# Kernel optimization log

Hardware: AMD Instinct MI355X
Metric: run time of the kernel (lower is better)

## Reference

```python
import jax, jax.numpy as jnp
import numpy as np

N_ATOMS = 100000
N_PAIRS = 3200000
N_PROP = 16
N_BASIS = 10
W = 16  # MLP width for pp/pi/ii nodes


def setup_inputs() -> dict:
    key = jax.random.key(0)
    ks = jax.random.split(key, 16)
    s = 0.1
    inp = {
        "ind_2": jax.random.randint(ks[0], (N_PAIRS, 2), 0, N_ATOMS),
        "p1": jax.random.normal(ks[1], (N_ATOMS, N_PROP), dtype=jnp.float32),
        "basis": jax.random.normal(ks[2], (N_PAIRS, N_BASIS), dtype=jnp.float32),
        # pp_pre: [16,16], bias=True
        "Wpre0": jax.random.normal(ks[3], (N_PROP, W), dtype=jnp.float32) * s,
        "bpre0": jnp.zeros((W,), dtype=jnp.float32),
        "Wpre1": jax.random.normal(ks[4], (W, W), dtype=jnp.float32) * s,
        "bpre1": jnp.zeros((W,), dtype=jnp.float32),
        # pi: input 2*W -> W -> W*n_basis, bias=True
        "Wpi0": jax.random.normal(ks[5], (2 * W, W), dtype=jnp.float32) * s,
        "bpi0": jnp.zeros((W,), dtype=jnp.float32),
        "Wpi1": jax.random.normal(ks[6], (W, W * N_BASIS), dtype=jnp.float32) * s,
        "bpi1": jnp.zeros((W * N_BASIS,), dtype=jnp.float32),
        # ii: [16,16], bias=False
        "Wii0": jax.random.normal(ks[7], (W, W), dtype=jnp.float32) * s,
        "Wii1": jax.random.normal(ks[8], (W, W), dtype=jnp.float32) * s,
        # pp_post: [16,16], bias=False
        "Wpost0": jax.random.normal(ks[9], (W, W), dtype=jnp.float32) * s,
        "Wpost1": jax.random.normal(ks[10], (W, W), dtype=jnp.float32) * s,
    }
    return inp


def reference(ind_2, p1, basis, Wpre0, bpre0, Wpre1, bpre1,
              Wpi0, bpi0, Wpi1, bpi1, Wii0, Wii1, Wpost0, Wpost1):
    act = jnp.tanh
    n_atoms = p1.shape[0]
    # pp_pre: per-atom FF (activation on every dense, bias=True)
    p1_in = act(p1 @ Wpre0 + bpre0)
    p1_in = act(p1_in @ Wpre1 + bpre1)
    # PI: gather pair endpoints, concat, MLP, contract with radial basis
    h = jnp.concatenate([p1_in[ind_2[:, 0]], p1_in[ind_2[:, 1]]], axis=-1)  # (P, 2W)
    h = act(h @ Wpi0 + bpi0)                                                # (P, W)
    h = act(h @ Wpi1 + bpi1)                                                # (P, W*n_basis)
    h = h.reshape(h.shape[0], -1, basis.shape[-1])                          # (P, W, n_basis)
    i_pair = jnp.einsum('pcb,pb->pc', h, basis)                             # (P, W)
    # II: pair-mixing FF (bias=False)
    i_pair = act(i_pair @ Wii0)
    i_pair = act(i_pair @ Wii1)
    # IP: scatter-sum pair features back to atoms at ind_2[:,0]
    p_sum = jax.ops.segment_sum(i_pair, ind_2[:, 0], num_segments=n_atoms)  # (A, W)
    # pp_post (bias=False)
    p1_new = act(p_sum @ Wpost0)
    p1_new = act(p1_new @ Wpost1)
    return (p1_new, i_pair)
```

## Files before the change

### kernel.cpp

```cpp
#include <hip/hip_runtime.h>

#define N_ATOMS 100000
#define N_PAIRS 3200000
#define N_PROP 16
#define N_BASIS 10
#define W 16
#define NSUP (N_PAIRS / 32)
#define SCAN_BLK 1024
#define NB ((N_ATOMS + SCAN_BLK - 1) / SCAN_BLK)
#define SC 2.88539008177792681f

typedef short  s16x8  __attribute__((ext_vector_type(8)));
typedef float  f32x4  __attribute__((ext_vector_type(4)));
typedef float  f32x16 __attribute__((ext_vector_type(16)));

__device__ __forceinline__ float tanh_pre(float y) {
    float e = __builtin_amdgcn_exp2f(y);
    return 1.0f - 2.0f * __builtin_amdgcn_rcpf(e + 1.0f);
}
__device__ __forceinline__ float fast_tanh(float x) {
    float e = __builtin_amdgcn_exp2f(x * SC);
    return 1.0f - 2.0f * __builtin_amdgcn_rcpf(e + 1.0f);
}
__device__ __forceinline__ unsigned short bf16r(float f) {
    union { float f; unsigned u; } v; v.f = f;
    unsigned r = v.u + 0x7FFFu + ((v.u >> 16) & 1u);
    return (unsigned short)(r >> 16);
}
__device__ __forceinline__ unsigned cvt_pk_bf16(float a, float b) {
    unsigned r;
    asm("v_cvt_pk_bf16_f32 %0, %1, %2" : "=v"(r) : "v"(a), "v"(b));
    return r;
}
__device__ __forceinline__ float bitf(unsigned u) {
    union { unsigned u; float f; } v; v.u = u; return v.f;
}
__device__ __forceinline__ void nt_store4(float* p, float a, float b, float c, float d) {
    f32x4 v = {a, b, c, d};
    __builtin_nontemporal_store(v, reinterpret_cast<f32x4*>(p));
}

__global__ __launch_bounds__(256) void k_pp_pre(
    const float* __restrict__ p1,
    const float* __restrict__ W0, const float* __restrict__ b0,
    const float* __restrict__ W1, const float* __restrict__ b1,
    const float* __restrict__ Wpi0, const float* __restrict__ bpi0,
    float* __restrict__ ytop, float* __restrict__ ybot)
{
    int a = blockIdx.x * 256 + threadIdx.x;
    if (a >= N_ATOMS) return;
    const float4* src = reinterpret_cast<const float4*>(p1 + (size_t)a * N_PROP);
    float4 v0 = src[0], v1 = src[1], v2 = src[2], v3 = src[3];
    float x[N_PROP] = {v0.x,v0.y,v0.z,v0.w, v1.x,v1.y,v1.z,v1.w,
                       v2.x,v2.y,v2.z,v2.w, v3.x,v3.y,v3.z,v3.w};
    float h[W];
#pragma unroll
    for (int c = 0; c < W; ++c) h[c] = b0[c];
#pragma unroll
    for (int k = 0; k < N_PROP; ++k)
#pragma unroll
        for (int c = 0; c < W; ++c) h[c] += x[k] * W0[k*W + c];
#pragma unroll
    for (int c = 0; c < W; ++c) h[c] = fast_tanh(h[c]);
    float y[W];
#pragma unroll
    for (int c = 0; c < W; ++c) y[c] = b1[c];
#pragma unroll
    for (int k = 0; k < W; ++k)
#pragma unroll
        for (int c = 0; c < W; ++c) y[c] += h[k] * W1[k*W + c];
    float t[W];
#pragma unroll
    for (int c = 0; c < W; ++c) t[c] = fast_tanh(y[c]);

    float yt[W], yb[W];
#pragma unroll
    for (int c = 0; c < W; ++c) { yt[c] = bpi0[c]; yb[c] = 0.0f; }
#pragma unroll
    for (int k = 0; k < W; ++k)
#pragma unroll
        for (int c = 0; c < W; ++c) {
            yt[c] += t[k] * Wpi0[k*W + c];
            yb[c] += t[k] * Wpi0[(W + k)*W + c];
        }
    float4* dt = reinterpret_cast<float4*>(ytop + (size_t)a * W);
    float4* db = reinterpret_cast<float4*>(ybot + (size_t)a * W);
#pragma unroll
    for (int q = 0; q < 4; ++q) {
        dt[q] = make_float4(SC*yt[4*q], SC*yt[4*q+1], SC*yt[4*q+2], SC*yt[4*q+3]);
        db[q] = make_float4(SC*yb[4*q], SC*yb[4*q+1], SC*yb[4*q+2], SC*yb[4*q+3]);
    }
}

template<int USE_RANK>
__global__ __launch_bounds__(256) void k_pair_mfma(
    const int*   __restrict__ ind2,
    const float* __restrict__ basis,
    const float* __restrict__ ytop,
    const float* __restrict__ ybot,
    const float* __restrict__ Wpi1, const float* __restrict__ bpi1,
    const float* __restrict__ Wii0, const float* __restrict__ Wii1,
    float* __restrict__ i_pair_out,
    const unsigned* __restrict__ starts,
    const unsigned* __restrict__ rank,
    unsigned* __restrict__ cursor,
    float* __restrict__ svals)
{
    __shared__ s16x8 aw_lds[5][2][32];
    __shared__ s16x8 ab_lds[5][2][32];

    const int lane = threadIdx.x & 63;
    const int wv   = threadIdx.x >> 6;
    const int col  = lane & 31;
    const int h    = lane >> 5;

    for (int e = threadIdx.x; e < 320; e += 256) {
        int T = e >> 6, hh = (e >> 5) & 1, row = e & 31;
        int colW = (4*(row >> 3) + (row & 3)) * N_BASIS + 2*T + ((row >> 2) & 1);
        s16x8 wfrag, bfrag;
#pragma unroll
        for (int j = 0; j < 8; ++j) {
            int k = 8*hh + j;
            wfrag[j] = (short)bf16r(SC * Wpi1[k*(W*N_BASIS) + colW]);
            bfrag[j] = (short)((k == 0) ? bf16r(SC * bpi1[colW]) : 0);
        }
        aw_lds[T][hh][row] = wfrag;
        ab_lds[T][hh][row] = bfrag;
    }

    s16x8 a3, a4;
#pragma unroll
    for (int j = 0; j < 8; ++j) {
        int k = 8*h + j;
        a3[j] = (short)(col < W ? bf16r(SC * Wii0[k*W + col]) : 0);
        a4[j] = (short)(col < W ? bf16r(SC * Wii1[k*W + col]) : 0);
    }
    s16x8 Bones = {0,0,0,0,0,0,0,0};
    if (h == 0) Bones[0] = (short)0x3F80;

    __syncthreads();

    const int stride = gridDim.x * 4;
    int sup = blockIdx.x * 4 + wv;
    if (sup >= NSUP) return;
    const int2* ind2v = reinterpret_cast<const int2*>(ind2);

    int2 ij = ind2v[(size_t)sup * 32 + col];
    f32x4 yt0 = *reinterpret_cast<const f32x4*>(ytop + (size_t)ij.x * W + 8*h);
    f32x4 yt1 = *reinterpret_cast<const f32x4*>(ytop + (size_t)ij.x * W + 8*h + 4);
    f32x4 yb0 = *reinterpret_cast<const f32x4*>(ybot + (size_t)ij.y * W + 8*h);
    f32x4 yb1 = *reinterpret_cast<const f32x4*>(ybot + (size_t)ij.y * W + 8*h + 4);

    for (; sup < NSUP; sup += stride) {
        const int p = sup * 32 + col;
        const int nsup = (sup + stride < NSUP) ? (sup + stride) : sup;

        int2 nij = ind2v[(size_t)nsup * 32 + col];

        float h0[8];
#pragma unroll
        for (int j = 0; j < 4; ++j) h0[j]     = tanh_pre(yt0[j] + yb0[j]);
#pragma unroll
        for (int j = 0; j < 4; ++j) h0[4 + j] = tanh_pre(yt1[j] + yb1[j]);
        unsigned w0h = cvt_pk_bf16(h0[0], h0[1]);
        unsigned w1h = cvt_pk_bf16(h0[2], h0[3]);
        unsigned w2h = cvt_pk_bf16(h0[4], h0[5]);
        unsigned w3h = cvt_pk_bf16(h0[6], h0[7]);
        unsigned w0l = cvt_pk_bf16(h0[0] - bitf(w0h << 16), h0[1] - bitf(w0h & 0xFFFF0000u));
        unsigned w1l = cvt_pk_bf16(h0[2] - bitf(w1h << 16), h0[3] - bitf(w1h & 0xFFFF0000u));
        unsigned w2l = cvt_pk_bf16(h0[4] - bitf(w2h << 16), h0[5] - bitf(w2h & 0xFFFF0000u));
        unsigned w3l = cvt_pk_bf16(h0[6] - bitf(w3h << 16), h0[7] - bitf(w3h & 0xFFFF0000u));
        union { unsigned u[4]; s16x8 v; } BH, BL;
        BH.u[0] = w0h; BH.u[1] = w1h; BH.u[2] = w2h; BH.u[3] = w3h;
        BL.u[0] = w0l; BL.u[1] = w1l; BL.u[2] = w2l; BL.u[3] = w3l;
        s16x8 B2h = BH.v, B2l = BL.v;

        const float2* bb = reinterpret_cast<const float2*>(basis + (size_t)p * N_BASIS);
        float bsel[5];
#pragma unroll
        for (int q = 0; q < 5; ++q) {
            float2 t2 = bb[q];
            bsel[q] = h ? t2.y : t2.x;
        }

        float v[16];
#pragma unroll
        for (int i = 0; i < 16; ++i) v[i] = 0.0f;
#pragma unroll
        for (int T = 0; T < 5; ++T) {
            s16x8 af = aw_lds[T][h][col];
            s16x8 ab = ab_lds[T][h][col];
            f32x16 z = {0.0f};
            z = __builtin_amdgcn_mfma_f32_32x32x16_bf16(ab, Bones, z, 0, 0, 0);
            z = __builtin_amdgcn_mfma_f32_32x32x16_bf16(af, B2h,  z, 0, 0, 0);
            z = __builtin_amdgcn_mfma_f32_32x32x16_bf16(af, B2l,  z, 0, 0, 0);
#pragma unroll
            for (int i = 0; i < 16; ++i)
                v[i] += tanh_pre(z[i]) * bsel[T];
        }

        f32x4 nyt0 = *reinterpret_cast<const f32x4*>(ytop + (size_t)nij.x * W + 8*h);
        f32x4 nyt1 = *reinterpret_cast<const f32x4*>(ytop + (size_t)nij.x * W + 8*h + 4);
        f32x4 nyb0 = *reinterpret_cast<const f32x4*>(ybot + (size_t)nij.y * W + 8*h);
        f32x4 nyb1 = *reinterpret_cast<const f32x4*>(ybot + (size_t)nij.y * W + 8*h + 4);

        float own[8], snd[8];
        if (h == 0) {
#pragma unroll
            for (int j = 0; j < 8; ++j) { own[j] = v[j]; snd[j] = v[8 + j]; }
        } else {
#pragma unroll
            for (int j = 0; j < 8; ++j) { own[j] = v[8 + j]; snd[j] = v[j]; }
        }
        float vf[8];
#pragma unroll
        for (int j = 0; j < 8; ++j) vf[j] = own[j] + __shfl_xor(snd[j], 32);

        union { unsigned u[4]; s16x8 v; } B3u;
        B3u.u[0] = cvt_pk_bf16(vf[0], vf[1]);
        B3u.u[1] = cvt_pk_bf16(vf[2], vf[3]);
        B3u.u[2] = cvt_pk_bf16(vf[4], vf[5]);
        B3u.u[3] = cvt_pk_bf16(vf[6], vf[7]);
        f32x16 ua = {0.0f};
        ua = __builtin_amdgcn_mfma_f32_32x32x16_bf16(a3, B3u.v, ua, 0, 0, 0);
        float u[8];
#pragma unroll
        for (int i = 0; i < 8; ++i) u[i] = tanh_pre(ua[i]);

        float uo[4], us[4];
        if (h == 0) {
#pragma unroll
            for (int j = 0; j < 4; ++j) { uo[j] = u[j]; us[j] = u[4 + j]; }
        } else {
#pragma unroll
            for (int j = 0; j < 4; ++j) { uo[j] = u[4 + j]; us[j] = u[j]; }
        }
        float ur[4];
#pragma unroll
        for (int j = 0; j < 4; ++j) ur[j] = __shfl_xor(us[j], 32);
        union { unsigned u[4]; s16x8 v; } B4u;
        if (h == 0) {
            B4u.u[0] = cvt_pk_bf16(uo[0], uo[1]);
            B4u.u[1] = cvt_pk_bf16(uo[2], uo[3]);
            B4u.u[2] = cvt_pk_bf16(ur[0], ur[1]);
            B4u.u[3] = cvt_pk_bf16(ur[2], ur[3]);
        } else {
            B4u.u[0] = cvt_pk_bf16(ur[0], ur[1]);
            B4u.u[1] = cvt_pk_bf16(ur[2], ur[3]);
            B4u.u[2] = cvt_pk_bf16(uo[0], uo[1]);
            B4u.u[3] = cvt_pk_bf16(uo[2], uo[3]);
        }
        f32x16 wa = {0.0f};
        wa = __builtin_amdgcn_mfma_f32_32x32x16_bf16(a4, B4u.v, wa, 0, 0, 0);
        float wq[8];
#pragma unroll
        for (int i = 0; i < 8; ++i) wq[i] = tanh_pre(wa[i]);

        const int off1 = h ? 4 : 0;
        const int off2 = h ? 12 : 8;
        float* ob = i_pair_out + (size_t)p * W;
        nt_store4(ob + off1, wq[0], wq[1], wq[2], wq[3]);
        nt_store4(ob + off2, wq[4], wq[5], wq[6], wq[7]);

        unsigned pos;
        if (USE_RANK) {
            pos = starts[ij.x] + rank[p];
        } else {
            unsigned pp = 0;
            if (h == 0) pp = atomicAdd(&cursor[ij.x], 1u);
            pos = (unsigned)__shfl((int)pp, col);
        }
        float* sb = svals + (size_t)pos * W;
        nt_store4(sb + off1, wq[0], wq[1], wq[2], wq[3]);
        nt_store4(sb + off2, wq[4], wq[5], wq[6], wq[7]);

        ij = nij;
        yt0 = nyt0; yt1 = nyt1; yb0 = nyb0; yb1 = nyb1;
    }
}

__global__ __launch_bounds__(256) void k_count(const int* __restrict__ ind2,
                                               unsigned* __restrict__ counts,
                                               unsigned* __restrict__ rank)
{
    int p = blockIdx.x * 256 + threadIdx.x;
    if (p >= N_PAIRS) return;
    rank[p] = atomicAdd(&counts[ind2[2*p]], 1u);
}

__global__ __launch_bounds__(SCAN_BLK) void k_scanA(const unsigned* __restrict__ counts,
                                                    unsigned* __restrict__ starts,
                                                    unsigned* __restrict__ bsum)
{
    __shared__ unsigned sc[SCAN_BLK];
    int a = blockIdx.x * SCAN_BLK + threadIdx.x;
    unsigned c = (a < N_ATOMS) ? counts[a] : 0u;
    sc[threadIdx.x] = c;
    __syncthreads();
    for (int off = 1; off < SCAN_BLK; off <<= 1) {
        unsigned v = sc[threadIdx.x];
        unsigned add = (threadIdx.x >= off) ? sc[threadIdx.x - off] : 0u;
        __syncthreads();
        sc[threadIdx.x] = v + add;
        __syncthreads();
    }
    if (a < N_ATOMS) starts[a] = sc[threadIdx.x] - c;
    if (threadIdx.x == SCAN_BLK - 1) bsum[blockIdx.x] = sc[SCAN_BLK - 1];
}

__global__ __launch_bounds__(128) void k_scanB(const unsigned* __restrict__ bsum,
                                               unsigned* __restrict__ boff)
{
    __shared__ unsigned s[128];
    int t = threadIdx.x;
    unsigned v = (t < NB) ? bsum[t] : 0u;
    s[t] = v;
    __syncthreads();
    for (int off = 1; off < 128; off <<= 1) {
        unsigned x = s[t];
        unsigned add = (t >= off) ? s[t - off] : 0u;
        __syncthreads();
        s[t] = x + add;
        __syncthreads();
    }
    if (t < NB) boff[t] = s[t] - v;
}

__global__ __launch_bounds__(SCAN_BLK) void k_scanC(unsigned* __restrict__ starts,
                                                    const unsigned* __restrict__ boff,
                                                    unsigned* __restrict__ cursor)
{
    int a = blockIdx.x * SCAN_BLK + threadIdx.x;
    if (a >= N_ATOMS) return;
    unsigned s = starts[a] + boff[blockIdx.x];
    starts[a] = s;
    cursor[a] = s;
}

__global__ __launch_bounds__(256) void k_reduce_stream(const unsigned* __restrict__ starts,
                                                       const unsigned* __restrict__ counts,
                                                       const float* __restrict__ svals,
                                                       float* __restrict__ p_sum)
{
    int a = blockIdx.x * 4 + (threadIdx.x >> 6);
    if (a >= N_ATOMS) return;
    int lane = threadIdx.x & 63;
    int c = lane & 15, q = lane >> 4;
    unsigned n = counts[a], st = starts[a];
    float acc = 0.0f;
    for (unsigned k = q; k < n; k += 4)
        acc += svals[(size_t)(st + k) * W + c];
    acc += __shfl_xor(acc, 16);
    acc += __shfl_xor(acc, 32);
    if (q == 0) p_sum[(size_t)a * W + c] = acc;
}

__global__ __launch_bounds__(256) void k_pp_post(
    const float* __restrict__ p_sum,
    const float* __restrict__ W0, const float* __restrict__ W1,
    float* __restrict__ p1_new)
{
    int a = blockIdx.x * 256 + threadIdx.x;
    if (a >= N_ATOMS) return;
    const float4* src = reinterpret_cast<const float4*>(p_sum + (size_t)a * W);
    float4 v0 = src[0], v1 = src[1], v2 = src[2], v3 = src[3];
    float x[W] = {v0.x,v0.y,v0.z,v0.w, v1.x,v1.y,v1.z,v1.w,
                  v2.x,v2.y,v2.z,v2.w, v3.x,v3.y,v3.z,v3.w};
    float h[W];
#pragma unroll
    for (int c = 0; c < W; ++c) h[c] = 0.0f;
#pragma unroll
    for (int k = 0; k < W; ++k)
#pragma unroll
        for (int c = 0; c < W; ++c) h[c] += x[k] * W0[k*W + c];
#pragma unroll
    for (int c = 0; c < W; ++c) h[c] = fast_tanh(h[c]);
    float y[W];
#pragma unroll
    for (int c = 0; c < W; ++c) y[c] = 0.0f;
#pragma unroll
    for (int k = 0; k < W; ++k)
#pragma unroll
        for (int c = 0; c < W; ++c) y[c] += h[k] * W1[k*W + c];
    float4* dst = reinterpret_cast<float4*>(p1_new + (size_t)a * W);
    dst[0] = make_float4(fast_tanh(y[0]),  fast_tanh(y[1]),  fast_tanh(y[2]),  fast_tanh(y[3]));
    dst[1] = make_float4(fast_tanh(y[4]),  fast_tanh(y[5]),  fast_tanh(y[6]),  fast_tanh(y[7]));
    dst[2] = make_float4(fast_tanh(y[8]),  fast_tanh(y[9]),  fast_tanh(y[10]), fast_tanh(y[11]));
    dst[3] = make_float4(fast_tanh(y[12]), fast_tanh(y[13]), fast_tanh(y[14]), fast_tanh(y[15]));
}

extern "C" void kernel_launch(void* const* d_in, const int* in_sizes, int n_in,
                              void* d_out, int out_size, void* d_ws, size_t ws_size,
                              hipStream_t stream) {
    const int*   ind2   = (const int*)d_in[0];
    const float* p1     = (const float*)d_in[1];
    const float* basis  = (const float*)d_in[2];
    const float* Wpre0  = (const float*)d_in[3];
    const float* bpre0  = (const float*)d_in[4];
    const float* Wpre1  = (const float*)d_in[5];
    const float* bpre1  = (const float*)d_in[6];
    const float* Wpi0   = (const float*)d_in[7];
    const float* bpi0   = (const float*)d_in[8];
    const float* Wpi1   = (const float*)d_in[9];
    const float* bpi1   = (const float*)d_in[10];
    const float* Wii0   = (const float*)d_in[11];
    const float* Wii1   = (const float*)d_in[12];
    const float* Wpost0 = (const float*)d_in[13];
    const float* Wpost1 = (const float*)d_in[14];

    float* out    = (float*)d_out;
    float* p1_new = out;
    float* i_pair = out + (size_t)N_ATOMS * W;

    char* ws = (char*)d_ws;
    float*    ytop   = (float*)ws;                                ws += (size_t)N_ATOMS * W * 4;
    float*    ybot   = (float*)ws;                                ws += (size_t)N_ATOMS * W * 4;
    float*    p_sum  = (float*)ws;                                ws += (size_t)N_ATOMS * W * 4;
    unsigned* counts = (unsigned*)ws;                             ws += (size_t)N_ATOMS * 4;
    unsigned* starts = (unsigned*)ws;                             ws += (size_t)N_ATOMS * 4;
    unsigned* cursor = (unsigned*)ws;                             ws += (size_t)N_ATOMS * 4;
    unsigned* bsum   = (unsigned*)ws;                             ws += 1024 * 4;
    unsigned* boff   = (unsigned*)ws;                             ws += 1024 * 4;
    float*    svals  = (float*)ws;                                ws += (size_t)N_PAIRS * W * 4;
    unsigned* rank   = (unsigned*)ws;                             ws += (size_t)N_PAIRS * 4;

    int use_rank = (ws_size >= (size_t)(ws - (char*)d_ws));

    hipMemsetAsync(counts, 0, (size_t)N_ATOMS * sizeof(unsigned), stream);
    k_pp_pre<<<(N_ATOMS + 255) / 256, 256, 0, stream>>>(p1, Wpre0, bpre0, Wpre1, bpre1,
                                                        Wpi0, bpi0, ytop, ybot);
    k_count<<<(N_PAIRS + 255) / 256, 256, 0, stream>>>(ind2, counts, use_rank ? rank : cursor);
    k_scanA<<<NB, SCAN_BLK, 0, stream>>>(counts, starts, bsum);
    k_scanB<<<1, 128, 0, stream>>>(bsum, boff);
    k_scanC<<<NB, SCAN_BLK, 0, stream>>>(starts, boff, cursor);

    if (use_rank) {
        k_pair_mfma<1><<<2560, 256, 0, stream>>>(ind2, basis, ytop, ybot,
                                                 Wpi1, bpi1, Wii0, Wii1,
                                                 i_pair, starts, rank, cursor, svals);
    } else {
        k_pair_mfma<0><<<2560, 256, 0, stream>>>(ind2, basis, ytop, ybot,
                                                 Wpi1, bpi1, Wii0, Wii1,
                                                 i_pair, starts, rank, cursor, svals);
    }
    k_reduce_stream<<<(N_ATOMS + 3) / 4, 256, 0, stream>>>(starts, counts, svals, p_sum);
    k_pp_post<<<(N_ATOMS + 255) / 256, 256, 0, stream>>>(p_sum, Wpost0, Wpost1, p1_new);
}
```

Before: 548.4 us.

## Transpose MFMA outputs via shuffles for row-contiguous stores; vectorize count and reduce

The pair kernel now shuffles MFMA output fragments across lanes so each group of four lanes writes one full 64-byte row of i_pair and svals, instead of scattered 16-byte pieces. k_count handles two pairs per thread with an int4 load and a paired rank store. k_reduce_stream reads float4 chunks with 16 pairs in flight per wave and reduces them with xor-shuffles. The aim is better store and load coalescing, paid for with extra shuffle and select instructions in the hot loop.

```diff
diff --git a/kernel.cpp b/kernel.cpp
--- a/kernel.cpp
+++ b/kernel.cpp
@@ -34,10 +34,6 @@
 }
 __device__ __forceinline__ float bitf(unsigned u) {
     union { unsigned u; float f; } v; v.u = u; return v.f;
-}
-__device__ __forceinline__ void nt_store4(float* p, float a, float b, float c, float d) {
-    f32x4 v = {a, b, c, d};
-    __builtin_nontemporal_store(v, reinterpret_cast<f32x4*>(p));
 }
 
 __global__ __launch_bounds__(256) void k_pp_pre(
@@ -152,7 +148,8 @@
     f32x4 yb1 = *reinterpret_cast<const f32x4*>(ybot + (size_t)ij.y * W + 8*h + 4);
 
     for (; sup < NSUP; sup += stride) {
-        const int p = sup * 32 + col;
+        const int p0 = sup * 32;
+        const int p  = p0 + col;
         const int nsup = (sup + stride < NSUP) ? (sup + stride) : sup;
 
         int2 nij = ind2v[(size_t)nsup * 32 + col];
@@ -256,12 +253,6 @@
 #pragma unroll
         for (int i = 0; i < 8; ++i) wq[i] = tanh_pre(wa[i]);
 
-        const int off1 = h ? 4 : 0;
-        const int off2 = h ? 12 : 8;
-        float* ob = i_pair_out + (size_t)p * W;
-        nt_store4(ob + off1, wq[0], wq[1], wq[2], wq[3]);
-        nt_store4(ob + off2, wq[4], wq[5], wq[6], wq[7]);
-
         unsigned pos;
         if (USE_RANK) {
             pos = starts[ij.x] + rank[p];
@@ -270,9 +261,26 @@
             if (h == 0) pp = atomicAdd(&cursor[ij.x], 1u);
             pos = (unsigned)__shfl((int)pp, col);
         }
-        float* sb = svals + (size_t)pos * W;
-        nt_store4(sb + off1, wq[0], wq[1], wq[2], wq[3]);
-        nt_store4(sb + off2, wq[4], wq[5], wq[6], wq[7]);
+
+        const int rk0 = lane & 15;
+        const int q   = lane >> 4;
+#pragma unroll
+        for (int k = 0; k < 2; ++k) {
+            int row = 16*k + rk0;
+            int src = row + 32*(q & 1);
+            float vA0 = __shfl(wq[0], src), vA1 = __shfl(wq[1], src);
+            float vA2 = __shfl(wq[2], src), vA3 = __shfl(wq[3], src);
+            float vB0 = __shfl(wq[4], src), vB1 = __shfl(wq[5], src);
+            float vB2 = __shfl(wq[6], src), vB3 = __shfl(wq[7], src);
+            bool hiq = (q >= 2);
+            f32x4 val = { hiq ? vB0 : vA0, hiq ? vB1 : vA1,
+                          hiq ? vB2 : vA2, hiq ? vB3 : vA3 };
+            unsigned posr = (unsigned)__shfl((int)pos, row);
+            __builtin_nontemporal_store(val,
+                reinterpret_cast<f32x4*>(i_pair_out + (size_t)(p0 + row) * W + q*4));
+            __builtin_nontemporal_store(val,
+                reinterpret_cast<f32x4*>(svals + (size_t)posr * W + q*4));
+        }
 
         ij = nij;
         yt0 = nyt0; yt1 = nyt1; yb0 = nyb0; yb1 = nyb1;
@@ -283,9 +291,13 @@
                                                unsigned* __restrict__ counts,
                                                unsigned* __restrict__ rank)
 {
-    int p = blockIdx.x * 256 + threadIdx.x;
-    if (p >= N_PAIRS) return;
-    rank[p] = atomicAdd(&counts[ind2[2*p]], 1u);
+    int t = blockIdx.x * 256 + threadIdx.x;
+    if (t >= N_PAIRS / 2) return;
+    int4 ii = reinterpret_cast<const int4*>(ind2)[t];
+    unsigned r0 = atomicAdd(&counts[ii.x], 1u);
+    unsigned r1 = atomicAdd(&counts[ii.z], 1u);
+    uint2 rr; rr.x = r0; rr.y = r1;
+    *reinterpret_cast<uint2*>(rank + 2*t) = rr;
 }
 
 __global__ __launch_bounds__(SCAN_BLK) void k_scanA(const unsigned* __restrict__ counts,
@@ -345,14 +357,21 @@
     int a = blockIdx.x * 4 + (threadIdx.x >> 6);
     if (a >= N_ATOMS) return;
     int lane = threadIdx.x & 63;
-    int c = lane & 15, q = lane >> 4;
+    int c4 = lane & 3;
+    int q  = lane >> 2;
     unsigned n = counts[a], st = starts[a];
-    float acc = 0.0f;
-    for (unsigned k = q; k < n; k += 4)
-        acc += svals[(size_t)(st + k) * W + c];
-    acc += __shfl_xor(acc, 16);
-    acc += __shfl_xor(acc, 32);
-    if (q == 0) p_sum[(size_t)a * W + c] = acc;
+    f32x4 acc = {0.f, 0.f, 0.f, 0.f};
+    for (unsigned k = q; k < n; k += 16)
+        acc += *reinterpret_cast<const f32x4*>(svals + (size_t)(st + k) * W + c4*4);
+#pragma unroll
+    for (int off = 4; off < 64; off <<= 1) {
+        acc[0] += __shfl_xor(acc[0], off);
+        acc[1] += __shfl_xor(acc[1], off);
+        acc[2] += __shfl_xor(acc[2], off);
+        acc[3] += __shfl_xor(acc[3], off);
+    }
+    if (lane < 4)
+        *reinterpret_cast<f32x4*>(p_sum + (size_t)a * W + lane*4) = acc;
 }
 
 __global__ __launch_bounds__(256) void k_pp_post(
@@ -429,7 +448,7 @@
     hipMemsetAsync(counts, 0, (size_t)N_ATOMS * sizeof(unsigned), stream);
     k_pp_pre<<<(N_ATOMS + 255) / 256, 256, 0, stream>>>(p1, Wpre0, bpre0, Wpre1, bpre1,
                                                         Wpi0, bpi0, ytop, ybot);
-    k_count<<<(N_PAIRS + 255) / 256, 256, 0, stream>>>(ind2, counts, use_rank ? rank : cursor);
+    k_count<<<(N_PAIRS / 2 + 255) / 256, 256, 0, stream>>>(ind2, counts, use_rank ? rank : cursor);
     k_scanA<<<NB, SCAN_BLK, 0, stream>>>(counts, starts, bsum);
     k_scanB<<<1, 128, 0, stream>>>(bsum, boff);
     k_scanC<<<NB, SCAN_BLK, 0, stream>>>(starts, boff, cursor);
```

After: 484.7 us. 1.13x faster.
